# Kernel tuning notes

Hardware: AMD Instinct MI355X
Metric: run time of the kernel (lower is better)

Reference implementation:

```python
import jax, jax.numpy as jnp
import numpy as np

HIDDEN = 4096
N_HEADS = 32
HEAD_DIM = HIDDEN // N_HEADS
MAX_POS = 2048
ROPE_BASE = 10000.0


def _rope_tables(head_dim, max_pos):
    inv_freq = 1.0 / (ROPE_BASE ** (np.arange(0, head_dim, 2, dtype=np.float32) / head_dim))
    t = np.arange(max_pos, dtype=np.float32)
    freqs = np.einsum('i,j->ij', t, inv_freq)          # [max_pos, head_dim//2]
    emb = np.concatenate([freqs, freqs], axis=-1)       # [max_pos, head_dim]
    return jnp.asarray(np.cos(emb)), jnp.asarray(np.sin(emb))


def _rotate_half(x):
    x1, x2 = jnp.split(x, 2, axis=-1)
    return jnp.concatenate([-x2, x1], axis=-1)


def setup_inputs() -> dict:
    key = jax.random.key(0)
    ks = jax.random.split(key, 5)
    B, S = 1, 2048
    hidden_states = jax.random.normal(ks[0], (B, S, HIDDEN), dtype=jnp.float32)
    # additive causal mask (0 on/below diagonal, large negative above)
    causal = jnp.triu(jnp.full((S, S), -1e9, dtype=jnp.float32), k=1)
    attention_mask = causal[None, None, :, :]
    scale = 0.02
    wq = jax.random.normal(ks[1], (HIDDEN, HIDDEN), dtype=jnp.float32) * scale
    wk = jax.random.normal(ks[2], (HIDDEN, HIDDEN), dtype=jnp.float32) * scale
    wv = jax.random.normal(ks[3], (HIDDEN, HIDDEN), dtype=jnp.float32) * scale
    wo = jax.random.normal(ks[4], (HIDDEN, HIDDEN), dtype=jnp.float32) * scale
    position_ids = jnp.arange(S, dtype=jnp.int64 if jax.config.jax_enable_x64 else jnp.int32)[None, :]
    return {"hidden_states": hidden_states, "attention_mask": attention_mask,
            "wq": wq, "wk": wk, "wv": wv, "wo": wo, "position_ids": position_ids}


def reference(hidden_states, attention_mask, wq, wk, wv, wo, position_ids):
    B, S, H = hidden_states.shape
    cos_tab, sin_tab = _rope_tables(HEAD_DIM, MAX_POS)

    def shape_heads(x):  # [B,S,H] -> [B,nH,S,hd]
        return x.reshape(B, S, N_HEADS, HEAD_DIM).transpose(0, 2, 1, 3)

    # QKV projections (torch Linear: x @ W.T, no bias)
    q = shape_heads(hidden_states @ wq.T)
    k = shape_heads(hidden_states @ wk.T)
    v = shape_heads(hidden_states @ wv.T)

    # RoPE
    cos = cos_tab[position_ids][:, None, :, :]  # [B,1,S,hd]
    sin = sin_tab[position_ids][:, None, :, :]
    q = q * cos + _rotate_half(q) * sin
    k = k * cos + _rotate_half(k) * sin

    # scaled dot-product attention
    scale = 1.0 / jnp.sqrt(jnp.float32(HEAD_DIM))
    scores = jnp.einsum('bhqd,bhkd->bhqk', q, k) * scale
    scores = scores + attention_mask  # broadcast over heads
    scores = jnp.maximum(scores, jnp.finfo(scores.dtype).min)
    probs = jax.nn.softmax(scores, axis=-1)
    attn = jnp.einsum('bhqk,bhkd->bhqd', probs, v)

    # merge heads, output projection
    attn = attn.transpose(0, 2, 1, 3).reshape(B, S, H)
    return attn @ wo.T
```

## Files before the change

### kernel.cpp

```cpp
#include <hip/hip_runtime.h>

typedef __bf16 bf16x8 __attribute__((ext_vector_type(8)));
typedef float f32x4 __attribute__((ext_vector_type(4)));

__device__ __forceinline__ ushort f2bf(float f) {
  uint u = __builtin_bit_cast(uint, f);
  u = (u + 0x7fffu + ((u >> 16) & 1u)) >> 16;
  return (ushort)u;
}
__device__ __forceinline__ ushort f2bf_fast(float f) {
  uint u = __builtin_bit_cast(uint, f);
  return (ushort)((u + 0x8000u) >> 16);
}
__device__ __forceinline__ float bf2f(ushort h) {
  uint u = ((uint)h) << 16;
  return __builtin_bit_cast(float, u);
}
__device__ __forceinline__ float ex2(float x) {
  return __builtin_amdgcn_exp2f(x);
}

__device__ __forceinline__ void gload16(const ushort* g, ushort* l) {
  __builtin_amdgcn_global_load_lds(
      (const __attribute__((address_space(1))) unsigned int*)(const void*)g,
      (__attribute__((address_space(3))) unsigned int*)(void*)l, 16, 0, 0);
}

__global__ void cvt_f32_bf16_k(const float* __restrict__ in, ushort* __restrict__ out, int n4) {
  int i = blockIdx.x * blockDim.x + threadIdx.x;
  if (i >= n4) return;
  float4 v = reinterpret_cast<const float4*>(in)[i];
  ushort4 o;
  o.x = f2bf(v.x); o.y = f2bf(v.y); o.z = f2bf(v.z); o.w = f2bf(v.w);
  reinterpret_cast<ushort4*>(out)[i] = o;
}

__global__ void rope_tables_k(float* __restrict__ cosT, float* __restrict__ sinT) {
  int i = blockIdx.x * 256 + threadIdx.x;
  int p = i >> 6, j = i & 63;
  float inv = powf(10000.0f, -(float)j / 64.0f);
  float ang = (float)p * inv;
  cosT[i] = cosf(ang);
  sinT[i] = sinf(ang);
}

__global__ void rope_k(ushort* __restrict__ Q, ushort* __restrict__ K,
                       const float* __restrict__ cosT, const float* __restrict__ sinT,
                       const int* __restrict__ pos) {
  int idx = blockIdx.x * 256 + threadIdx.x;
  int s = idx >> 11;
  int rest = idx & 2047;
  int h = rest >> 6, d = rest & 63;
  int p = pos[s];
  float c = cosT[p * 64 + d], sn = sinT[p * 64 + d];
  size_t base = (size_t)s * 4096 + h * 128 + d;
  float q1 = bf2f(Q[base]), q2 = bf2f(Q[base + 64]);
  Q[base]      = f2bf(q1 * c - q2 * sn);
  Q[base + 64] = f2bf(q2 * c + q1 * sn);
  float k1 = bf2f(K[base]), k2 = bf2f(K[base + 64]);
  K[base]      = f2bf(k1 * c - k2 * sn);
  K[base + 64] = f2bf(k2 * c + k1 * sn);
}

template<typename TA, typename TW, int OMODE>
__global__ __launch_bounds__(256) void gemm_bt(const TA* __restrict__ A, const TW* __restrict__ W,
                                               void* __restrict__ Cout) {
  constexpr int K = 4096, N = 4096, NT = K / 64;
  constexpr bool BF = (sizeof(TA) == 2 && sizeof(TW) == 2);
  __shared__ ushort As[2][128 * 64];
  __shared__ ushort Ws[2][128 * 64];
  const int tid = threadIdx.x;
  const int w = tid >> 6, lane = tid & 63, g = lane >> 4, r = lane & 15;
  const int wr = w >> 1, wc = w & 1;
  const int id = blockIdx.x;
  const int xcd = id & 7, slot = id >> 3;
  const int nb = (xcd & 3) * 8 + (slot & 7);
  const int mb = (xcd >> 2) * 8 + (slot >> 3);
  const int m0 = mb * 128, n0 = nb * 128;

  auto stage = [&](int t, int b) {
    const int k0 = t * 64;
    if constexpr (BF) {
#pragma unroll
      for (int i = 0; i < 4; i++) {
        int r0 = (w * 4 + i) * 8;
        int row = r0 + (lane >> 3), c = lane & 7;
        int cs = (c ^ (row & 7)) * 8;
        gload16((const ushort*)A + (size_t)(m0 + row) * K + k0 + cs, &As[b][r0 * 64]);
        gload16((const ushort*)W + (size_t)(n0 + row) * K + k0 + cs, &Ws[b][r0 * 64]);
      }
    } else {
#pragma unroll
      for (int i = 0; i < 4; i++) {
        int li = tid + i * 256, row = li >> 3, c = li & 7;
        int cs = (c ^ (row & 7)) * 8;
        const float* srcA = (const float*)A + (size_t)(m0 + row) * K + k0 + cs;
        float4 a0 = *reinterpret_cast<const float4*>(srcA);
        float4 a1 = *reinterpret_cast<const float4*>(srcA + 4);
        ushort oa[8] = {f2bf(a0.x), f2bf(a0.y), f2bf(a0.z), f2bf(a0.w),
                        f2bf(a1.x), f2bf(a1.y), f2bf(a1.z), f2bf(a1.w)};
        *reinterpret_cast<uint4*>(&As[b][row * 64 + c * 8]) = *reinterpret_cast<uint4*>(oa);
        const float* srcW = (const float*)W + (size_t)(n0 + row) * K + k0 + cs;
        float4 w0 = *reinterpret_cast<const float4*>(srcW);
        float4 w1 = *reinterpret_cast<const float4*>(srcW + 4);
        ushort ow[8] = {f2bf(w0.x), f2bf(w0.y), f2bf(w0.z), f2bf(w0.w),
                        f2bf(w1.x), f2bf(w1.y), f2bf(w1.z), f2bf(w1.w)};
        *reinterpret_cast<uint4*>(&Ws[b][row * 64 + c * 8]) = *reinterpret_cast<uint4*>(ow);
      }
    }
  };

  f32x4 acc[4][4];
#pragma unroll
  for (int i = 0; i < 4; i++)
#pragma unroll
    for (int j = 0; j < 4; j++) acc[i][j] = f32x4{0.f, 0.f, 0.f, 0.f};

  stage(0, 0);
  __syncthreads();

#pragma unroll 1
  for (int t = 0; t < NT; ++t) {
    const int buf = t & 1;
    if (t + 1 < NT) stage(t + 1, buf ^ 1);
#pragma unroll
    for (int kk = 0; kk < 2; kk++) {
      bf16x8 af[4], bfr[4];
#pragma unroll
      for (int mi = 0; mi < 4; mi++) {
        int row = wr * 64 + mi * 16 + r;
        af[mi] = *reinterpret_cast<const bf16x8*>((const char*)&As[buf][0] + row * 128 + (((g + kk * 4) ^ (r & 7)) * 16));
      }
#pragma unroll
      for (int nj = 0; nj < 4; nj++) {
        int row = wc * 64 + nj * 16 + r;
        bfr[nj] = *reinterpret_cast<const bf16x8*>((const char*)&Ws[buf][0] + row * 128 + (((g + kk * 4) ^ (r & 7)) * 16));
      }
#pragma unroll
      for (int mi = 0; mi < 4; mi++)
#pragma unroll
        for (int nj = 0; nj < 4; nj++)
          acc[mi][nj] = __builtin_amdgcn_mfma_f32_16x16x32_bf16(af[mi], bfr[nj], acc[mi][nj], 0, 0, 0);
    }
    __syncthreads();
  }

  if constexpr (OMODE == 0) {
    float* C = (float*)Cout;
#pragma unroll
    for (int mi = 0; mi < 4; mi++)
#pragma unroll
      for (int nj = 0; nj < 4; nj++)
#pragma unroll
        for (int j = 0; j < 4; j++) {
          int row = m0 + wr * 64 + mi * 16 + g * 4 + j;
          int col = n0 + wc * 64 + nj * 16 + r;
          C[(size_t)row * N + col] = acc[mi][nj][j];
        }
  } else if constexpr (OMODE == 1) {
    ushort* C = (ushort*)Cout;
#pragma unroll
    for (int mi = 0; mi < 4; mi++)
#pragma unroll
      for (int nj = 0; nj < 4; nj++)
#pragma unroll
        for (int j = 0; j < 4; j++) {
          int row = m0 + wr * 64 + mi * 16 + g * 4 + j;
          int col = n0 + wc * 64 + nj * 16 + r;
          C[(size_t)row * N + col] = f2bf(acc[mi][nj][j]);
        }
  } else {
    ushort* C = (ushort*)Cout;
#pragma unroll
    for (int mi = 0; mi < 4; mi++)
#pragma unroll
      for (int nj = 0; nj < 4; nj++) {
        int col = n0 + wc * 64 + nj * 16 + r;
        int row0 = m0 + wr * 64 + mi * 16 + g * 4;
        ushort4 v;
        v.x = f2bf(acc[mi][nj][0]); v.y = f2bf(acc[mi][nj][1]);
        v.z = f2bf(acc[mi][nj][2]); v.w = f2bf(acc[mi][nj][3]);
        *reinterpret_cast<ushort4*>(C + (size_t)col * 2048 + row0) = v;
      }
  }
}

__global__ __launch_bounds__(256) void attn_fwd(const ushort* __restrict__ Q, const ushort* __restrict__ K,
                                                const ushort* __restrict__ Vt, ushort* __restrict__ O) {
  constexpr int S = 2048, HD = 4096;
  constexpr float SC2 = 0.12753102f;
  constexpr float THR = 90.50967f;
  __shared__ ushort Ks[2][64 * 128];
  __shared__ ushort Vs[2][128 * 64];
  __shared__ ushort Ps[4][16 * 64];
  const int id = blockIdx.x;
  const int xcd = id & 7, slot = id >> 3;
  const int h = xcd * 4 + (slot & 3);
  const int qx = slot >> 2;
  const int tid = threadIdx.x;
  const int w = tid >> 6, lane = tid & 63, g = lane >> 4, r = lane & 15;
  const int kRow = lane >> 4, kC = lane & 15;
  const int vRow = lane >> 3, vC = lane & 7;

#pragma unroll 1
  for (int pass = 0; pass < 2; ++pass) {
    const int qtile = pass ? (31 - qx) : qx;
    const int qbase = qtile * 64;
    const int nt = qtile + 1;

    bf16x8 qf[4];
    {
      const int qrow = qbase + w * 16 + r;
#pragma unroll
      for (int dc = 0; dc < 4; dc++)
        qf[dc] = *reinterpret_cast<const bf16x8*>(Q + (size_t)qrow * HD + h * 128 + dc * 32 + g * 8);
    }

    f32x4 o[8];
#pragma unroll
    for (int i = 0; i < 8; i++) o[i] = f32x4{0.f, 0.f, 0.f, 0.f};
    float m[4] = {-3e38f, -3e38f, -3e38f, -3e38f};
    float l[4] = {0.f, 0.f, 0.f, 0.f};

    __syncthreads();
#pragma unroll
    for (int i = 0; i < 4; i++) {
      int kr0 = (w * 4 + i) * 4, krow = kr0 + kRow;
      gload16(K + (size_t)krow * HD + h * 128 + (kC ^ (krow & 7)) * 8, &Ks[0][kr0 * 128]);
      int vr0 = (w * 4 + i) * 8, vrow = vr0 + vRow;
      gload16(Vt + (size_t)(h * 128 + vrow) * S + (vC ^ (vrow & 7)) * 8, &Vs[0][vr0 * 64]);
    }

#pragma unroll 1
    for (int t = 0; t < nt; ++t) {
      const int kv0 = t * 64;
      const int buf = t & 1;
      __syncthreads();
      if (t + 1 < nt) {
        const int kvn = kv0 + 64;
#pragma unroll
        for (int i = 0; i < 4; i++) {
          int kr0 = (w * 4 + i) * 4, krow = kr0 + kRow;
          gload16(K + (size_t)(kvn + krow) * HD + h * 128 + (kC ^ (krow & 7)) * 8, &Ks[buf ^ 1][kr0 * 128]);
          int vr0 = (w * 4 + i) * 8, vrow = vr0 + vRow;
          gload16(Vt + (size_t)(h * 128 + vrow) * S + kvn + (vC ^ (vrow & 7)) * 8, &Vs[buf ^ 1][vr0 * 64]);
        }
      }

      f32x4 sc[4];
      __builtin_amdgcn_s_setprio(1);
#pragma unroll
      for (int c = 0; c < 4; c++) {
        f32x4 tacc = f32x4{0.f, 0.f, 0.f, 0.f};
        const int krow = c * 16 + r;
        const char* kb = (const char*)&Ks[buf][0] + krow * 256;
#pragma unroll
        for (int dc = 0; dc < 4; dc++) {
          bf16x8 kf = *reinterpret_cast<const bf16x8*>(kb + ((dc * 64 + g * 16) ^ ((krow & 7) << 4)));
          tacc = __builtin_amdgcn_mfma_f32_16x16x32_bf16(qf[dc], kf, tacc, 0, 0, 0);
        }
        sc[c] = tacc;
      }
      __builtin_amdgcn_s_setprio(0);

      if (t == nt - 1) {
#pragma unroll
        for (int c = 0; c < 4; c++) {
          int kvg = kv0 + c * 16 + r;
#pragma unroll
          for (int j = 0; j < 4; j++) {
            int qg = qbase + w * 16 + g * 4 + j;
            if (kvg > qg) sc[c][j] = -3e38f;
          }
        }
      }

      float pm[4];
#pragma unroll
      for (int j = 0; j < 4; j++)
        pm[j] = fmaxf(fmaxf(sc[0][j], sc[1][j]), fmaxf(sc[2][j], sc[3][j]));
#pragma unroll
      for (int st = 1; st < 16; st <<= 1) {
        float t0 = __shfl_xor(pm[0], st);
        float t1 = __shfl_xor(pm[1], st);
        float t2 = __shfl_xor(pm[2], st);
        float t3 = __shfl_xor(pm[3], st);
        pm[0] = fmaxf(pm[0], t0); pm[1] = fmaxf(pm[1], t1);
        pm[2] = fmaxf(pm[2], t2); pm[3] = fmaxf(pm[3], t3);
      }

      bool ok = (pm[0] - m[0] <= THR) && (pm[1] - m[1] <= THR) &&
                (pm[2] - m[2] <= THR) && (pm[3] - m[3] <= THR);
      if (!__all(ok)) {
#pragma unroll
        for (int j = 0; j < 4; j++) {
          float mn = fmaxf(m[j], pm[j]);
          float alpha = ex2((m[j] - mn) * SC2);
          m[j] = mn;
          l[j] *= alpha;
#pragma unroll
          for (int dc = 0; dc < 8; dc++) o[dc][j] *= alpha;
        }
      }

      float ps[4];
      char* pb = (char*)&Ps[w][0];
#pragma unroll
      for (int j = 0; j < 4; j++) {
        float mb = m[j] * SC2;
        float p0 = ex2(__builtin_fmaf(sc[0][j], SC2, -mb));
        float p1 = ex2(__builtin_fmaf(sc[1][j], SC2, -mb));
        float p2 = ex2(__builtin_fmaf(sc[2][j], SC2, -mb));
        float p3 = ex2(__builtin_fmaf(sc[3][j], SC2, -mb));
        ps[j] = (p0 + p1) + (p2 + p3);
        int ql = g * 4 + j;
        char* pr = pb + (size_t)ql * 128;
        uint sw = (ql & 7) << 4;
        *reinterpret_cast<ushort*>(pr + ((0 * 32 + r * 2) ^ sw)) = f2bf_fast(p0);
        *reinterpret_cast<ushort*>(pr + ((1 * 32 + r * 2) ^ sw)) = f2bf_fast(p1);
        *reinterpret_cast<ushort*>(pr + ((2 * 32 + r * 2) ^ sw)) = f2bf_fast(p2);
        *reinterpret_cast<ushort*>(pr + ((3 * 32 + r * 2) ^ sw)) = f2bf_fast(p3);
      }

      __builtin_amdgcn_s_setprio(1);
#pragma unroll
      for (int c2 = 0; c2 < 2; c2++) {
        bf16x8 pf = *reinterpret_cast<const bf16x8*>(pb + (size_t)r * 128 + ((c2 * 64 + g * 16) ^ ((r & 7) << 4)));
#pragma unroll
        for (int dc = 0; dc < 8; dc++) {
          const int vrow = dc * 16 + r;
          bf16x8 vf = *reinterpret_cast<const bf16x8*>((const char*)&Vs[buf][0] + vrow * 128 + ((c2 * 64 + g * 16) ^ ((vrow & 7) << 4)));
          o[dc] = __builtin_amdgcn_mfma_f32_16x16x32_bf16(pf, vf, o[dc], 0, 0, 0);
        }
      }
      __builtin_amdgcn_s_setprio(0);

#pragma unroll
      for (int st = 1; st < 16; st <<= 1) {
        float t0 = __shfl_xor(ps[0], st);
        float t1 = __shfl_xor(ps[1], st);
        float t2 = __shfl_xor(ps[2], st);
        float t3 = __shfl_xor(ps[3], st);
        ps[0] += t0; ps[1] += t1; ps[2] += t2; ps[3] += t3;
      }
#pragma unroll
      for (int j = 0; j < 4; j++) l[j] += ps[j];
    }

    float rl[4];
#pragma unroll
    for (int j = 0; j < 4; j++) rl[j] = __builtin_amdgcn_rcpf(l[j]);
#pragma unroll
    for (int dc = 0; dc < 8; dc++)
#pragma unroll
      for (int j = 0; j < 4; j++) {
        float v = o[dc][j] * rl[j];
        O[(size_t)(qbase + w * 16 + g * 4 + j) * HD + h * 128 + dc * 16 + r] = f2bf(v);
      }
  }
}

extern "C" void kernel_launch(void* const* d_in, const int* in_sizes, int n_in,
                              void* d_out, int out_size, void* d_ws, size_t ws_size,
                              hipStream_t stream) {
  const float* X  = (const float*)d_in[0];
  const float* Wq = (const float*)d_in[2];
  const float* Wk = (const float*)d_in[3];
  const float* Wv = (const float*)d_in[4];
  const float* Wo = (const float*)d_in[5];
  const int* pos  = (const int*)d_in[6];
  float* out = (float*)d_out;
  char* ws = (char*)d_ws;
  const size_t MB = 1024ull * 1024ull;

  float*  tabC = (float*)(ws + 0);
  float*  tabS = (float*)(ws + 512 * 1024);
  ushort* Qb   = (ushort*)(ws + 1 * MB);
  ushort* Kb   = (ushort*)(ws + 17 * MB);
  ushort* Vt   = (ushort*)(ws + 33 * MB);
  ushort* Ab   = (ushort*)(ws + 49 * MB);
  ushort* Xb   = (ushort*)(ws + 65 * MB);
  ushort* Wb   = (ushort*)(ws + 81 * MB);
  const bool fast = ws_size >= 113 * MB;

  rope_tables_k<<<512, 256, 0, stream>>>(tabC, tabS);

  if (fast) {
    cvt_f32_bf16_k<<<8192, 256, 0, stream>>>(X, Xb, 2097152);
    cvt_f32_bf16_k<<<16384, 256, 0, stream>>>(Wq, Wb, 4194304);
    gemm_bt<ushort, ushort, 1><<<512, 256, 0, stream>>>(Xb, Wb, Qb);
    cvt_f32_bf16_k<<<16384, 256, 0, stream>>>(Wk, Wb, 4194304);
    gemm_bt<ushort, ushort, 1><<<512, 256, 0, stream>>>(Xb, Wb, Kb);
    cvt_f32_bf16_k<<<16384, 256, 0, stream>>>(Wv, Wb, 4194304);
    gemm_bt<ushort, ushort, 2><<<512, 256, 0, stream>>>(Xb, Wb, Vt);
    rope_k<<<16384, 256, 0, stream>>>(Qb, Kb, tabC, tabS, pos);
    attn_fwd<<<512, 256, 0, stream>>>(Qb, Kb, Vt, Ab);
    cvt_f32_bf16_k<<<16384, 256, 0, stream>>>(Wo, Wb, 4194304);
    gemm_bt<ushort, ushort, 0><<<512, 256, 0, stream>>>(Ab, Wb, out);
  } else {
    gemm_bt<float, float, 1><<<512, 256, 0, stream>>>(X, Wq, Qb);
    gemm_bt<float, float, 1><<<512, 256, 0, stream>>>(X, Wk, Kb);
    gemm_bt<float, float, 2><<<512, 256, 0, stream>>>(X, Wv, Vt);
    rope_k<<<16384, 256, 0, stream>>>(Qb, Kb, tabC, tabS, pos);
    attn_fwd<<<512, 256, 0, stream>>>(Qb, Kb, Vt, Ab);
    gemm_bt<ushort, float, 0><<<512, 256, 0, stream>>>(Ab, Wo, out);
  }
}
```

Before: 467.3 us.

## Process both causal query tiles concurrently in one 512-thread attention block

The attention kernel goes from 256 to 512 threads per block. The two wave groups handle the paired query tiles (qx and 31-qx) at the same time instead of one after the other, and they share a single stream of K/V tiles staged through LDS. This halves the K/V loads that the two passes used to repeat for the shorter tile, and it doubles the waves in flight. In exchange, the group with the short tile sits idle through the remaining iterations but still has to hit every barrier. The larger Ps buffer and the higher per-block register budget may also limit occupancy.

```diff
diff --git a/kernel.cpp b/kernel.cpp
--- a/kernel.cpp
+++ b/kernel.cpp
@@ -185,68 +185,63 @@
   }
 }
 
-__global__ __launch_bounds__(256) void attn_fwd(const ushort* __restrict__ Q, const ushort* __restrict__ K,
+__global__ __launch_bounds__(512) void attn_fwd(const ushort* __restrict__ Q, const ushort* __restrict__ K,
                                                 const ushort* __restrict__ Vt, ushort* __restrict__ O) {
   constexpr int S = 2048, HD = 4096;
   constexpr float SC2 = 0.12753102f;
   constexpr float THR = 90.50967f;
   __shared__ ushort Ks[2][64 * 128];
   __shared__ ushort Vs[2][128 * 64];
-  __shared__ ushort Ps[4][16 * 64];
+  __shared__ ushort Ps[8][16 * 64];
   const int id = blockIdx.x;
   const int xcd = id & 7, slot = id >> 3;
   const int h = xcd * 4 + (slot & 3);
   const int qx = slot >> 2;
   const int tid = threadIdx.x;
   const int w = tid >> 6, lane = tid & 63, g = lane >> 4, r = lane & 15;
+  const int grp = w >> 2, wl = w & 3;
+  const int qtile = grp ? (31 - qx) : qx;
+  const int qbase = qtile * 64;
+  const int ntg = qtile + 1;
+  const int ntmax = 32 - qx;
   const int kRow = lane >> 4, kC = lane & 15;
   const int vRow = lane >> 3, vC = lane & 7;
 
+  bf16x8 qf[4];
+  {
+    const int qrow = qbase + wl * 16 + r;
+#pragma unroll
+    for (int dc = 0; dc < 4; dc++)
+      qf[dc] = *reinterpret_cast<const bf16x8*>(Q + (size_t)qrow * HD + h * 128 + dc * 32 + g * 8);
+  }
+
+  f32x4 o[8];
+#pragma unroll
+  for (int i = 0; i < 8; i++) o[i] = f32x4{0.f, 0.f, 0.f, 0.f};
+  float m[4] = {-3e38f, -3e38f, -3e38f, -3e38f};
+  float l[4] = {0.f, 0.f, 0.f, 0.f};
+
+  auto stage = [&](int t, int b) {
+    const int kv0 = t * 64;
+#pragma unroll
+    for (int i = 0; i < 2; i++) {
+      int kr0 = (w * 2 + i) * 4, krow = kr0 + kRow;
+      gload16(K + (size_t)(kv0 + krow) * HD + h * 128 + (kC ^ (krow & 7)) * 8, &Ks[b][kr0 * 128]);
+      int vr0 = (w * 2 + i) * 8, vrow = vr0 + vRow;
+      gload16(Vt + (size_t)(h * 128 + vrow) * S + kv0 + (vC ^ (vrow & 7)) * 8, &Vs[b][vr0 * 64]);
+    }
+  };
+
+  stage(0, 0);
+
 #pragma unroll 1
-  for (int pass = 0; pass < 2; ++pass) {
-    const int qtile = pass ? (31 - qx) : qx;
-    const int qbase = qtile * 64;
-    const int nt = qtile + 1;
-
-    bf16x8 qf[4];
-    {
-      const int qrow = qbase + w * 16 + r;
-#pragma unroll
-      for (int dc = 0; dc < 4; dc++)
-        qf[dc] = *reinterpret_cast<const bf16x8*>(Q + (size_t)qrow * HD + h * 128 + dc * 32 + g * 8);
-    }
-
-    f32x4 o[8];
-#pragma unroll
-    for (int i = 0; i < 8; i++) o[i] = f32x4{0.f, 0.f, 0.f, 0.f};
-    float m[4] = {-3e38f, -3e38f, -3e38f, -3e38f};
-    float l[4] = {0.f, 0.f, 0.f, 0.f};
-
+  for (int t = 0; t < ntmax; ++t) {
+    const int kv0 = t * 64;
+    const int buf = t & 1;
     __syncthreads();
-#pragma unroll
-    for (int i = 0; i < 4; i++) {
-      int kr0 = (w * 4 + i) * 4, krow = kr0 + kRow;
-      gload16(K + (size_t)krow * HD + h * 128 + (kC ^ (krow & 7)) * 8, &Ks[0][kr0 * 128]);
-      int vr0 = (w * 4 + i) * 8, vrow = vr0 + vRow;
-      gload16(Vt + (size_t)(h * 128 + vrow) * S + (vC ^ (vrow & 7)) * 8, &Vs[0][vr0 * 64]);
-    }
-
-#pragma unroll 1
-    for (int t = 0; t < nt; ++t) {
-      const int kv0 = t * 64;
-      const int buf = t & 1;
-      __syncthreads();
-      if (t + 1 < nt) {
-        const int kvn = kv0 + 64;
-#pragma unroll
-        for (int i = 0; i < 4; i++) {
-          int kr0 = (w * 4 + i) * 4, krow = kr0 + kRow;
-          gload16(K + (size_t)(kvn + krow) * HD + h * 128 + (kC ^ (krow & 7)) * 8, &Ks[buf ^ 1][kr0 * 128]);
-          int vr0 = (w * 4 + i) * 8, vrow = vr0 + vRow;
-          gload16(Vt + (size_t)(h * 128 + vrow) * S + kvn + (vC ^ (vrow & 7)) * 8, &Vs[buf ^ 1][vr0 * 64]);
-        }
-      }
-
+    if (t + 1 < ntmax) stage(t + 1, buf ^ 1);
+
+    if (t < ntg) {
       f32x4 sc[4];
       __builtin_amdgcn_s_setprio(1);
 #pragma unroll
@@ -263,13 +258,13 @@
       }
       __builtin_amdgcn_s_setprio(0);
 
-      if (t == nt - 1) {
+      if (t == ntg - 1) {
 #pragma unroll
         for (int c = 0; c < 4; c++) {
           int kvg = kv0 + c * 16 + r;
 #pragma unroll
           for (int j = 0; j < 4; j++) {
-            int qg = qbase + w * 16 + g * 4 + j;
+            int qg = qbase + wl * 16 + g * 4 + j;
             if (kvg > qg) sc[c][j] = -3e38f;
           }
         }
@@ -346,18 +341,18 @@
 #pragma unroll
       for (int j = 0; j < 4; j++) l[j] += ps[j];
     }
-
-    float rl[4];
-#pragma unroll
-    for (int j = 0; j < 4; j++) rl[j] = __builtin_amdgcn_rcpf(l[j]);
-#pragma unroll
-    for (int dc = 0; dc < 8; dc++)
-#pragma unroll
-      for (int j = 0; j < 4; j++) {
-        float v = o[dc][j] * rl[j];
-        O[(size_t)(qbase + w * 16 + g * 4 + j) * HD + h * 128 + dc * 16 + r] = f2bf(v);
-      }
   }
+
+  float rl[4];
+#pragma unroll
+  for (int j = 0; j < 4; j++) rl[j] = __builtin_amdgcn_rcpf(l[j]);
+#pragma unroll
+  for (int dc = 0; dc < 8; dc++)
+#pragma unroll
+    for (int j = 0; j < 4; j++) {
+      float v = o[dc][j] * rl[j];
+      O[(size_t)(qbase + wl * 16 + g * 4 + j) * HD + h * 128 + dc * 16 + r] = f2bf(v);
+    }
 }
 
 extern "C" void kernel_launch(void* const* d_in, const int* in_sizes, int n_in,
@@ -394,7 +389,7 @@
     cvt_f32_bf16_k<<<16384, 256, 0, stream>>>(Wv, Wb, 4194304);
     gemm_bt<ushort, ushort, 2><<<512, 256, 0, stream>>>(Xb, Wb, Vt);
     rope_k<<<16384, 256, 0, stream>>>(Qb, Kb, tabC, tabS, pos);
-    attn_fwd<<<512, 256, 0, stream>>>(Qb, Kb, Vt, Ab);
+    attn_fwd<<<512, 512, 0, stream>>>(Qb, Kb, Vt, Ab);
     cvt_f32_bf16_k<<<16384, 256, 0, stream>>>(Wo, Wb, 4194304);
     gemm_bt<ushort, ushort, 0><<<512, 256, 0, stream>>>(Ab, Wb, out);
   } else {
@@ -402,7 +397,7 @@
     gemm_bt<float, float, 1><<<512, 256, 0, stream>>>(X, Wk, Kb);
     gemm_bt<float, float, 2><<<512, 256, 0, stream>>>(X, Wv, Vt);
     rope_k<<<16384, 256, 0, stream>>>(Qb, Kb, tabC, tabS, pos);
-    attn_fwd<<<512, 256, 0, stream>>>(Qb, Kb, Vt, Ab);
+    attn_fwd<<<512, 512, 0, stream>>>(Qb, Kb, Vt, Ab);
     gemm_bt<ushort, float, 0><<<512, 256, 0, stream>>>(Ab, Wo, out);
   }
 }
```

After: 488.6 us. 4.6% more time.

## Split attention into one q-tile per block and single-buffer K/V in LDS

Applied to the files above, without the earlier changes.

The attention kernel now launches 1024 blocks, each handling one query tile, instead of 512 blocks that each processed a paired short and long tile. Q tiles are scheduled longest first (qtile = 31 - index). K/V double buffering is replaced with a single LDS buffer that is loaded after the compute and waited on with vmcnt(0) plus a barrier. The smaller LDS footprint should allow more resident blocks per CU for latency hiding, at the cost of losing in-block overlap between loads and compute.

```diff
diff --git a/kernel.cpp b/kernel.cpp
--- a/kernel.cpp
+++ b/kernel.cpp
@@ -190,174 +190,168 @@
   constexpr int S = 2048, HD = 4096;
   constexpr float SC2 = 0.12753102f;
   constexpr float THR = 90.50967f;
-  __shared__ ushort Ks[2][64 * 128];
-  __shared__ ushort Vs[2][128 * 64];
+  __shared__ ushort Ks[64 * 128];
+  __shared__ ushort Vs[128 * 64];
   __shared__ ushort Ps[4][16 * 64];
   const int id = blockIdx.x;
-  const int xcd = id & 7, slot = id >> 3;
-  const int h = xcd * 4 + (slot & 3);
-  const int qx = slot >> 2;
+  const int xcd = id & 7, rest = id >> 3;
+  const int h = xcd * 4 + (rest & 3);
+  const int qtile = 31 - (rest >> 2);
+  const int qbase = qtile * 64;
+  const int nt = qtile + 1;
   const int tid = threadIdx.x;
   const int w = tid >> 6, lane = tid & 63, g = lane >> 4, r = lane & 15;
   const int kRow = lane >> 4, kC = lane & 15;
   const int vRow = lane >> 3, vC = lane & 7;
 
-#pragma unroll 1
-  for (int pass = 0; pass < 2; ++pass) {
-    const int qtile = pass ? (31 - qx) : qx;
-    const int qbase = qtile * 64;
-    const int nt = qtile + 1;
-
-    bf16x8 qf[4];
-    {
-      const int qrow = qbase + w * 16 + r;
-#pragma unroll
-      for (int dc = 0; dc < 4; dc++)
-        qf[dc] = *reinterpret_cast<const bf16x8*>(Q + (size_t)qrow * HD + h * 128 + dc * 32 + g * 8);
-    }
-
-    f32x4 o[8];
-#pragma unroll
-    for (int i = 0; i < 8; i++) o[i] = f32x4{0.f, 0.f, 0.f, 0.f};
-    float m[4] = {-3e38f, -3e38f, -3e38f, -3e38f};
-    float l[4] = {0.f, 0.f, 0.f, 0.f};
-
-    __syncthreads();
+  auto stage = [&](int t) {
+    const int kv0 = t * 64;
 #pragma unroll
     for (int i = 0; i < 4; i++) {
       int kr0 = (w * 4 + i) * 4, krow = kr0 + kRow;
-      gload16(K + (size_t)krow * HD + h * 128 + (kC ^ (krow & 7)) * 8, &Ks[0][kr0 * 128]);
+      gload16(K + (size_t)(kv0 + krow) * HD + h * 128 + (kC ^ (krow & 7)) * 8, &Ks[kr0 * 128]);
       int vr0 = (w * 4 + i) * 8, vrow = vr0 + vRow;
-      gload16(Vt + (size_t)(h * 128 + vrow) * S + (vC ^ (vrow & 7)) * 8, &Vs[0][vr0 * 64]);
-    }
+      gload16(Vt + (size_t)(h * 128 + vrow) * S + kv0 + (vC ^ (vrow & 7)) * 8, &Vs[vr0 * 64]);
+    }
+  };
+
+  bf16x8 qf[4];
+  {
+    const int qrow = qbase + w * 16 + r;
+#pragma unroll
+    for (int dc = 0; dc < 4; dc++)
+      qf[dc] = *reinterpret_cast<const bf16x8*>(Q + (size_t)qrow * HD + h * 128 + dc * 32 + g * 8);
+  }
+
+  f32x4 o[8];
+#pragma unroll
+  for (int i = 0; i < 8; i++) o[i] = f32x4{0.f, 0.f, 0.f, 0.f};
+  float m[4] = {-3e38f, -3e38f, -3e38f, -3e38f};
+  float l[4] = {0.f, 0.f, 0.f, 0.f};
+
+  stage(0);
 
 #pragma unroll 1
-    for (int t = 0; t < nt; ++t) {
-      const int kv0 = t * 64;
-      const int buf = t & 1;
-      __syncthreads();
-      if (t + 1 < nt) {
-        const int kvn = kv0 + 64;
-#pragma unroll
-        for (int i = 0; i < 4; i++) {
-          int kr0 = (w * 4 + i) * 4, krow = kr0 + kRow;
-          gload16(K + (size_t)(kvn + krow) * HD + h * 128 + (kC ^ (krow & 7)) * 8, &Ks[buf ^ 1][kr0 * 128]);
-          int vr0 = (w * 4 + i) * 8, vrow = vr0 + vRow;
-          gload16(Vt + (size_t)(h * 128 + vrow) * S + kvn + (vC ^ (vrow & 7)) * 8, &Vs[buf ^ 1][vr0 * 64]);
+  for (int t = 0; t < nt; ++t) {
+    const int kv0 = t * 64;
+    asm volatile("s_waitcnt vmcnt(0)" ::: "memory");
+    __builtin_amdgcn_sched_barrier(0);
+    __builtin_amdgcn_s_barrier();
+    __builtin_amdgcn_sched_barrier(0);
+
+    f32x4 sc[4];
+    __builtin_amdgcn_s_setprio(1);
+#pragma unroll
+    for (int c = 0; c < 4; c++) {
+      f32x4 tacc = f32x4{0.f, 0.f, 0.f, 0.f};
+      const int krow = c * 16 + r;
+      const char* kb = (const char*)&Ks[0] + krow * 256;
+#pragma unroll
+      for (int dc = 0; dc < 4; dc++) {
+        bf16x8 kf = *reinterpret_cast<const bf16x8*>(kb + ((dc * 64 + g * 16) ^ ((krow & 7) << 4)));
+        tacc = __builtin_amdgcn_mfma_f32_16x16x32_bf16(qf[dc], kf, tacc, 0, 0, 0);
+      }
+      sc[c] = tacc;
+    }
+    __builtin_amdgcn_s_setprio(0);
+
+    if (t == nt - 1) {
+#pragma unroll
+      for (int c = 0; c < 4; c++) {
+        int kvg = kv0 + c * 16 + r;
+#pragma unroll
+        for (int j = 0; j < 4; j++) {
+          int qg = qbase + w * 16 + g * 4 + j;
+          if (kvg > qg) sc[c][j] = -3e38f;
         }
       }
-
-      f32x4 sc[4];
-      __builtin_amdgcn_s_setprio(1);
-#pragma unroll
-      for (int c = 0; c < 4; c++) {
-        f32x4 tacc = f32x4{0.f, 0.f, 0.f, 0.f};
-        const int krow = c * 16 + r;
-        const char* kb = (const char*)&Ks[buf][0] + krow * 256;
-#pragma unroll
-        for (int dc = 0; dc < 4; dc++) {
-          bf16x8 kf = *reinterpret_cast<const bf16x8*>(kb + ((dc * 64 + g * 16) ^ ((krow & 7) << 4)));
-          tacc = __builtin_amdgcn_mfma_f32_16x16x32_bf16(qf[dc], kf, tacc, 0, 0, 0);
-        }
-        sc[c] = tacc;
-      }
-      __builtin_amdgcn_s_setprio(0);
-
-      if (t == nt - 1) {
-#pragma unroll
-        for (int c = 0; c < 4; c++) {
-          int kvg = kv0 + c * 16 + r;
-#pragma unroll
-          for (int j = 0; j < 4; j++) {
-            int qg = qbase + w * 16 + g * 4 + j;
-            if (kvg > qg) sc[c][j] = -3e38f;
-          }
-        }
-      }
-
-      float pm[4];
-#pragma unroll
-      for (int j = 0; j < 4; j++)
-        pm[j] = fmaxf(fmaxf(sc[0][j], sc[1][j]), fmaxf(sc[2][j], sc[3][j]));
-#pragma unroll
-      for (int st = 1; st < 16; st <<= 1) {
-        float t0 = __shfl_xor(pm[0], st);
-        float t1 = __shfl_xor(pm[1], st);
-        float t2 = __shfl_xor(pm[2], st);
-        float t3 = __shfl_xor(pm[3], st);
-        pm[0] = fmaxf(pm[0], t0); pm[1] = fmaxf(pm[1], t1);
-        pm[2] = fmaxf(pm[2], t2); pm[3] = fmaxf(pm[3], t3);
-      }
-
-      bool ok = (pm[0] - m[0] <= THR) && (pm[1] - m[1] <= THR) &&
-                (pm[2] - m[2] <= THR) && (pm[3] - m[3] <= THR);
-      if (!__all(ok)) {
-#pragma unroll
-        for (int j = 0; j < 4; j++) {
-          float mn = fmaxf(m[j], pm[j]);
-          float alpha = ex2((m[j] - mn) * SC2);
-          m[j] = mn;
-          l[j] *= alpha;
-#pragma unroll
-          for (int dc = 0; dc < 8; dc++) o[dc][j] *= alpha;
-        }
-      }
-
-      float ps[4];
-      char* pb = (char*)&Ps[w][0];
+    }
+
+    float pm[4];
+#pragma unroll
+    for (int j = 0; j < 4; j++)
+      pm[j] = fmaxf(fmaxf(sc[0][j], sc[1][j]), fmaxf(sc[2][j], sc[3][j]));
+#pragma unroll
+    for (int st = 1; st < 16; st <<= 1) {
+      float t0 = __shfl_xor(pm[0], st);
+      float t1 = __shfl_xor(pm[1], st);
+      float t2 = __shfl_xor(pm[2], st);
+      float t3 = __shfl_xor(pm[3], st);
+      pm[0] = fmaxf(pm[0], t0); pm[1] = fmaxf(pm[1], t1);
+      pm[2] = fmaxf(pm[2], t2); pm[3] = fmaxf(pm[3], t3);
+    }
+
+    bool ok = (pm[0] - m[0] <= THR) && (pm[1] - m[1] <= THR) &&
+              (pm[2] - m[2] <= THR) && (pm[3] - m[3] <= THR);
+    if (!__all(ok)) {
 #pragma unroll
       for (int j = 0; j < 4; j++) {
-        float mb = m[j] * SC2;
-        float p0 = ex2(__builtin_fmaf(sc[0][j], SC2, -mb));
-        float p1 = ex2(__builtin_fmaf(sc[1][j], SC2, -mb));
-        float p2 = ex2(__builtin_fmaf(sc[2][j], SC2, -mb));
-        float p3 = ex2(__builtin_fmaf(sc[3][j], SC2, -mb));
-        ps[j] = (p0 + p1) + (p2 + p3);
-        int ql = g * 4 + j;
-        char* pr = pb + (size_t)ql * 128;
-        uint sw = (ql & 7) << 4;
-        *reinterpret_cast<ushort*>(pr + ((0 * 32 + r * 2) ^ sw)) = f2bf_fast(p0);
-        *reinterpret_cast<ushort*>(pr + ((1 * 32 + r * 2) ^ sw)) = f2bf_fast(p1);
-        *reinterpret_cast<ushort*>(pr + ((2 * 32 + r * 2) ^ sw)) = f2bf_fast(p2);
-        *reinterpret_cast<ushort*>(pr + ((3 * 32 + r * 2) ^ sw)) = f2bf_fast(p3);
-      }
-
-      __builtin_amdgcn_s_setprio(1);
-#pragma unroll
-      for (int c2 = 0; c2 < 2; c2++) {
-        bf16x8 pf = *reinterpret_cast<const bf16x8*>(pb + (size_t)r * 128 + ((c2 * 64 + g * 16) ^ ((r & 7) << 4)));
-#pragma unroll
-        for (int dc = 0; dc < 8; dc++) {
-          const int vrow = dc * 16 + r;
-          bf16x8 vf = *reinterpret_cast<const bf16x8*>((const char*)&Vs[buf][0] + vrow * 128 + ((c2 * 64 + g * 16) ^ ((vrow & 7) << 4)));
-          o[dc] = __builtin_amdgcn_mfma_f32_16x16x32_bf16(pf, vf, o[dc], 0, 0, 0);
-        }
-      }
-      __builtin_amdgcn_s_setprio(0);
-
-#pragma unroll
-      for (int st = 1; st < 16; st <<= 1) {
-        float t0 = __shfl_xor(ps[0], st);
-        float t1 = __shfl_xor(ps[1], st);
-        float t2 = __shfl_xor(ps[2], st);
-        float t3 = __shfl_xor(ps[3], st);
-        ps[0] += t0; ps[1] += t1; ps[2] += t2; ps[3] += t3;
-      }
-#pragma unroll
-      for (int j = 0; j < 4; j++) l[j] += ps[j];
-    }
-
-    float rl[4];
-#pragma unroll
-    for (int j = 0; j < 4; j++) rl[j] = __builtin_amdgcn_rcpf(l[j]);
-#pragma unroll
-    for (int dc = 0; dc < 8; dc++)
-#pragma unroll
-      for (int j = 0; j < 4; j++) {
-        float v = o[dc][j] * rl[j];
-        O[(size_t)(qbase + w * 16 + g * 4 + j) * HD + h * 128 + dc * 16 + r] = f2bf(v);
-      }
+        float mn = fmaxf(m[j], pm[j]);
+        float alpha = ex2((m[j] - mn) * SC2);
+        m[j] = mn;
+        l[j] *= alpha;
+#pragma unroll
+        for (int dc = 0; dc < 8; dc++) o[dc][j] *= alpha;
+      }
+    }
+
+    float ps[4];
+    char* pb = (char*)&Ps[w][0];
+#pragma unroll
+    for (int j = 0; j < 4; j++) {
+      float mb = m[j] * SC2;
+      float p0 = ex2(__builtin_fmaf(sc[0][j], SC2, -mb));
+      float p1 = ex2(__builtin_fmaf(sc[1][j], SC2, -mb));
+      float p2 = ex2(__builtin_fmaf(sc[2][j], SC2, -mb));
+      float p3 = ex2(__builtin_fmaf(sc[3][j], SC2, -mb));
+      ps[j] = (p0 + p1) + (p2 + p3);
+      int ql = g * 4 + j;
+      char* pr = pb + (size_t)ql * 128;
+      uint sw = (ql & 7) << 4;
+      *reinterpret_cast<ushort*>(pr + ((0 * 32 + r * 2) ^ sw)) = f2bf_fast(p0);
+      *reinterpret_cast<ushort*>(pr + ((1 * 32 + r * 2) ^ sw)) = f2bf_fast(p1);
+      *reinterpret_cast<ushort*>(pr + ((2 * 32 + r * 2) ^ sw)) = f2bf_fast(p2);
+      *reinterpret_cast<ushort*>(pr + ((3 * 32 + r * 2) ^ sw)) = f2bf_fast(p3);
+    }
+
+    __builtin_amdgcn_s_setprio(1);
+#pragma unroll
+    for (int c2 = 0; c2 < 2; c2++) {
+      bf16x8 pf = *reinterpret_cast<const bf16x8*>(pb + (size_t)r * 128 + ((c2 * 64 + g * 16) ^ ((r & 7) << 4)));
+#pragma unroll
+      for (int dc = 0; dc < 8; dc++) {
+        const int vrow = dc * 16 + r;
+        bf16x8 vf = *reinterpret_cast<const bf16x8*>((const char*)&Vs[0] + vrow * 128 + ((c2 * 64 + g * 16) ^ ((vrow & 7) << 4)));
+        o[dc] = __builtin_amdgcn_mfma_f32_16x16x32_bf16(pf, vf, o[dc], 0, 0, 0);
+      }
+    }
+    __builtin_amdgcn_s_setprio(0);
+
+#pragma unroll
+    for (int st = 1; st < 16; st <<= 1) {
+      float t0 = __shfl_xor(ps[0], st);
+      float t1 = __shfl_xor(ps[1], st);
+      float t2 = __shfl_xor(ps[2], st);
+      float t3 = __shfl_xor(ps[3], st);
+      ps[0] += t0; ps[1] += t1; ps[2] += t2; ps[3] += t3;
+    }
+#pragma unroll
+    for (int j = 0; j < 4; j++) l[j] += ps[j];
+
+    __syncthreads();
+    if (t + 1 < nt) stage(t + 1);
   }
+
+  float rl[4];
+#pragma unroll
+  for (int j = 0; j < 4; j++) rl[j] = __builtin_amdgcn_rcpf(l[j]);
+#pragma unroll
+  for (int dc = 0; dc < 8; dc++)
+#pragma unroll
+    for (int j = 0; j < 4; j++) {
+      float v = o[dc][j] * rl[j];
+      O[(size_t)(qbase + w * 16 + g * 4 + j) * HD + h * 128 + dc * 16 + r] = f2bf(v);
+    }
 }
 
 extern "C" void kernel_launch(void* const* d_in, const int* in_sizes, int n_in,
@@ -394,7 +388,7 @@
     cvt_f32_bf16_k<<<16384, 256, 0, stream>>>(Wv, Wb, 4194304);
     gemm_bt<ushort, ushort, 2><<<512, 256, 0, stream>>>(Xb, Wb, Vt);
     rope_k<<<16384, 256, 0, stream>>>(Qb, Kb, tabC, tabS, pos);
-    attn_fwd<<<512, 256, 0, stream>>>(Qb, Kb, Vt, Ab);
+    attn_fwd<<<1024, 256, 0, stream>>>(Qb, Kb, Vt, Ab);
     cvt_f32_bf16_k<<<16384, 256, 0, stream>>>(Wo, Wb, 4194304);
     gemm_bt<ushort, ushort, 0><<<512, 256, 0, stream>>>(Ab, Wb, out);
   } else {
@@ -402,7 +396,7 @@
     gemm_bt<float, float, 1><<<512, 256, 0, stream>>>(X, Wk, Kb);
     gemm_bt<float, float, 2><<<512, 256, 0, stream>>>(X, Wv, Vt);
     rope_k<<<16384, 256, 0, stream>>>(Qb, Kb, tabC, tabS, pos);
-    attn_fwd<<<512, 256, 0, stream>>>(Qb, Kb, Vt, Ab);
+    attn_fwd<<<1024, 256, 0, stream>>>(Qb, Kb, Vt, Ab);
     gemm_bt<ushort, float, 0><<<512, 256, 0, stream>>>(Ab, Wo, out);
   }
 }
```

After: 466.3 us. About the same (-0.2%).
